# Kernel tuning notes

Hardware: AMD Instinct MI355X
Metric: run time of the kernel (lower is better)

## Reference

```python
import jax, jax.numpy as jnp
import numpy as np

WS = (7, 7)          # window size
SS = (3, 3)          # shift size
NUM_HEADS = 6


def _relative_position_index(ws):
    ch, cw = np.meshgrid(np.arange(ws[0]), np.arange(ws[1]), indexing='ij')
    coords = np.stack([ch, cw]).reshape(2, -1)           # [2, N]
    rel = coords[:, :, None] - coords[:, None, :]        # [2, N, N]
    rel = rel.transpose(1, 2, 0)
    rel[:, :, 0] += ws[0] - 1
    rel[:, :, 1] += ws[1] - 1
    rel[:, :, 0] *= 2 * ws[1] - 1
    return rel.sum(-1).reshape(-1)                       # [N*N]


def _shift_mask(pad_H, pad_W, ws, ss):
    # per-window additive mask [num_windows, N, N], -100 across shift regions
    img = np.zeros((pad_H, pad_W))
    h_slices = ((0, -ws[0]), (-ws[0], -ss[0]), (-ss[0], None))
    w_slices = ((0, -ws[1]), (-ws[1], -ss[1]), (-ss[1], None))
    cnt = 0
    for h in h_slices:
        for w in w_slices:
            img[h[0]:h[1], w[0]:w[1]] = cnt
            cnt += 1
    m = img.reshape(pad_H // ws[0], ws[0], pad_W // ws[1], ws[1])
    m = m.transpose(0, 2, 1, 3).reshape(-1, ws[0] * ws[1])   # [nW, N]
    diff = m[:, None, :] - m[:, :, None]
    return np.where(diff != 0, -100.0, 0.0).astype(np.float32)


def setup_inputs() -> dict:
    key = jax.random.key(0)
    ks = jax.random.split(key, 6)
    B, H, W, C = 16, 112, 112, 192
    return {
        'x': jax.random.normal(ks[0], (B, H, W, C), jnp.float32),
        'qkv_w': jax.random.normal(ks[1], (3 * C, C), jnp.float32) * (C ** -0.5),
        'qkv_b': jax.random.normal(ks[2], (3 * C,), jnp.float32) * 0.02,
        'proj_w': jax.random.normal(ks[3], (C, C), jnp.float32) * (C ** -0.5),
        'proj_b': jax.random.normal(ks[4], (C,), jnp.float32) * 0.02,
        'rel_bias_table': jax.random.normal(ks[5], ((2 * WS[0] - 1) * (2 * WS[1] - 1), NUM_HEADS), jnp.float32) * 0.02,
    }


def reference(x, qkv_w, qkv_b, proj_w, proj_b, rel_bias_table):
    B, H, W, C = x.shape
    ws, ss = WS, SS
    N = ws[0] * ws[1]
    hd = C // NUM_HEADS

    pad_r = (ws[1] - W % ws[1]) % ws[1]
    pad_b = (ws[0] - H % ws[0]) % ws[0]
    x = jnp.pad(x, ((0, 0), (0, pad_b), (0, pad_r), (0, 0)))
    pad_H, pad_W = H + pad_b, W + pad_r
    ss = (0 if ws[0] >= pad_H else ss[0], 0 if ws[1] >= pad_W else ss[1])
    shifted = sum(ss) > 0

    if shifted:
        x = jnp.roll(x, (-ss[0], -ss[1]), axis=(1, 2))

    nWh, nWw = pad_H // ws[0], pad_W // ws[1]
    nW = nWh * nWw
    # window partition -> [B*nW, N, C]
    x = x.reshape(B, nWh, ws[0], nWw, ws[1], C).transpose(0, 1, 3, 2, 4, 5).reshape(B * nW, N, C)

    qkv = x @ qkv_w.T + qkv_b                               # [B*nW, N, 3C]
    qkv = qkv.reshape(B * nW, N, 3, NUM_HEADS, hd).transpose(2, 0, 3, 1, 4)
    q, k, v = qkv[0], qkv[1], qkv[2]                        # [B*nW, h, N, hd]

    q = q * (hd ** -0.5)
    attn = jnp.einsum('whnd,whmd->whnm', q, k)              # [B*nW, h, N, N]

    rel_idx = _relative_position_index(ws)
    rel_bias = rel_bias_table[rel_idx].reshape(N, N, NUM_HEADS).transpose(2, 0, 1)
    attn = attn + rel_bias[None]

    if shifted:
        mask = jnp.asarray(_shift_mask(pad_H, pad_W, ws, ss))   # [nW, N, N]
        attn = attn.reshape(B, nW, NUM_HEADS, N, N) + mask[None, :, None]
        attn = attn.reshape(B * nW, NUM_HEADS, N, N)

    attn = jax.nn.softmax(attn, axis=-1)
    out = jnp.einsum('whnm,whmd->whnd', attn, v)            # [B*nW, h, N, hd]
    out = out.transpose(0, 2, 1, 3).reshape(B * nW, N, C)
    out = out @ proj_w.T + proj_b

    out = out.reshape(B, nWh, nWw, ws[0], ws[1], C).transpose(0, 1, 3, 2, 4, 5).reshape(B, pad_H, pad_W, C)
    if shifted:
        out = jnp.roll(out, (ss[0], ss[1]), axis=(1, 2))
    return out[:, :H, :W, :]
```

## Files before the change

### kernel.cpp

```cpp
#include <hip/hip_runtime.h>

typedef __bf16 bf16_t;
typedef __bf16 bf16x8 __attribute__((ext_vector_type(8)));
typedef __bf16 bf16x4 __attribute__((ext_vector_type(4)));
typedef float  f32x4  __attribute__((ext_vector_type(4)));

#define MFMA16(a,b,c) __builtin_amdgcn_mfma_f32_16x16x32_bf16((a),(b),(c),0,0,0)

#define REG_STRIDE 200
#define VT_STRIDE  68
#define REG_ELEMS  13056
#define SC_STRIDE  40
#define SC_CHUNK   640
#define BT_OFF     (REG_ELEMS + 6 * SC_CHUNK)
#define SMEM_ELEMS (BT_OFF + 1014)

#define WPROJ_OFF 110592
#define WTOTAL    147456

__global__ void convert_w_kernel(const float* __restrict__ qkv_w,
                                 const float* __restrict__ proj_w,
                                 bf16_t* __restrict__ wb) {
    const int i = (blockIdx.x * 256 + threadIdx.x) * 4;
    float4 f;
    if (i < WPROJ_OFF) f = *(const float4*)(qkv_w + i);
    else               f = *(const float4*)(proj_w + (i - WPROJ_OFF));
    bf16x4 v;
    v[0] = (bf16_t)f.x; v[1] = (bf16_t)f.y; v[2] = (bf16_t)f.z; v[3] = (bf16_t)f.w;
    *(bf16x4*)(wb + i) = v;
}

__device__ __forceinline__ void gemm64x32(const bf16_t* __restrict__ xa,
                                          const bf16_t* __restrict__ w0,
                                          const bf16_t* __restrict__ w1,
                                          f32x4 acc[4][2]) {
    bf16x8 b0 = *(const bf16x8*)(w0);
    bf16x8 b1 = *(const bf16x8*)(w1);
    bf16x8 n0 = *(const bf16x8*)(w0 + 32);
    bf16x8 n1 = *(const bf16x8*)(w1 + 32);
    #pragma unroll
    for (int ks = 0; ks < 6; ++ks) {
        bf16x8 m0, m1;
        if (ks < 4) {
            m0 = *(const bf16x8*)(w0 + (ks + 2) * 32);
            m1 = *(const bf16x8*)(w1 + (ks + 2) * 32);
        }
        #pragma unroll
        for (int mi = 0; mi < 4; ++mi) {
            const bf16x8 afr = *(const bf16x8*)(xa + (mi * 16) * REG_STRIDE + ks * 32);
            acc[mi][0] = MFMA16(afr, b0, acc[mi][0]);
            acc[mi][1] = MFMA16(afr, b1, acc[mi][1]);
        }
        b0 = n0; b1 = n1; n0 = m0; n1 = m1;
    }
}

__global__ __launch_bounds__(384, 5)
void swin_fused_kernel(const float* __restrict__ x,
                       const bf16_t* __restrict__ wbuf,
                       const float* __restrict__ qkv_b,
                       const float* __restrict__ proj_b,
                       const float* __restrict__ tbl,
                       float* __restrict__ out)
{
    __shared__ __align__(16) bf16_t smem[SMEM_ELEMS];
    bf16_t* region = smem;
    bf16_t* bt     = smem + BT_OFF;

    const int tid    = threadIdx.x;
    const int lane   = tid & 63;
    const int wave   = tid >> 6;
    const int lanelo = lane & 15;
    const int quad   = lane >> 4;

    bf16_t* sc = smem + REG_ELEMS + wave * SC_CHUNK;

    const int blk = blockIdx.x;
    const int b   = blk >> 8;
    const int wh  = (blk >> 4) & 15;
    const int ww  = blk & 15;
    const int rowbase = wh * 7 + 3;
    const int colbase = ww * 7 + 3;

    for (int i = tid; i < 1014; i += 384) bt[i] = (bf16_t)tbl[i];

    for (int idx = tid; idx < 64 * 48; idx += 384) {
        const int t  = idx / 48;
        const int c4 = (idx - t * 48) * 4;
        bf16x4 v4;
        if (t < 49) {
            int gr = rowbase + t / 7;  if (gr >= 112) gr -= 112;
            int gc = colbase + t % 7;  if (gc >= 112) gc -= 112;
            const float4 f = *(const float4*)(x + (((long)b * 112 + gr) * 112 + gc) * 192 + c4);
            v4[0] = (bf16_t)f.x; v4[1] = (bf16_t)f.y;
            v4[2] = (bf16_t)f.z; v4[3] = (bf16_t)f.w;
        } else {
            v4[0] = (bf16_t)0.0f; v4[1] = (bf16_t)0.0f;
            v4[2] = (bf16_t)0.0f; v4[3] = (bf16_t)0.0f;
        }
        *(bf16x4*)(region + t * REG_STRIDE + c4) = v4;
    }
    __syncthreads();

    const int h = wave;
    const bf16_t* xa = region + lanelo * REG_STRIDE + quad * 8;

    bf16x8 qa[4], kb[4];
    f32x4  vacc[4][2];
    {
        {
            const bf16_t* wb = wbuf + (0 * 192 + h * 32) * 192;
            f32x4 acc[4][2] = {};
            gemm64x32(xa, wb + lanelo * 192 + quad * 8, wb + (16 + lanelo) * 192 + quad * 8, acc);
            const float bias0 = qkv_b[0 * 192 + h * 32 + lanelo];
            const float bias1 = qkv_b[0 * 192 + h * 32 + 16 + lanelo];
            #pragma unroll
            for (int mi = 0; mi < 4; ++mi) {
                #pragma unroll
                for (int r = 0; r < 4; ++r) {
                    sc[(quad * 4 + r) * SC_STRIDE + lanelo]      = (bf16_t)(acc[mi][0][r] + bias0);
                    sc[(quad * 4 + r) * SC_STRIDE + 16 + lanelo] = (bf16_t)(acc[mi][1][r] + bias1);
                }
                qa[mi] = *(const bf16x8*)(sc + lanelo * SC_STRIDE + quad * 8);
            }
        }
        {
            const bf16_t* wb = wbuf + (1 * 192 + h * 32) * 192;
            f32x4 acc[4][2] = {};
            gemm64x32(xa, wb + lanelo * 192 + quad * 8, wb + (16 + lanelo) * 192 + quad * 8, acc);
            const float bias0 = qkv_b[1 * 192 + h * 32 + lanelo];
            const float bias1 = qkv_b[1 * 192 + h * 32 + 16 + lanelo];
            #pragma unroll
            for (int mi = 0; mi < 4; ++mi) {
                #pragma unroll
                for (int r = 0; r < 4; ++r) {
                    sc[(quad * 4 + r) * SC_STRIDE + lanelo]      = (bf16_t)(acc[mi][0][r] + bias0);
                    sc[(quad * 4 + r) * SC_STRIDE + 16 + lanelo] = (bf16_t)(acc[mi][1][r] + bias1);
                }
                kb[mi] = *(const bf16x8*)(sc + lanelo * SC_STRIDE + quad * 8);
            }
        }
        {
            const bf16_t* wb = wbuf + (2 * 192 + h * 32) * 192;
            f32x4 acc[4][2] = {};
            gemm64x32(xa, wb + lanelo * 192 + quad * 8, wb + (16 + lanelo) * 192 + quad * 8, acc);
            #pragma unroll
            for (int mi = 0; mi < 4; ++mi) {
                vacc[mi][0] = acc[mi][0];
                vacc[mi][1] = acc[mi][1];
            }
        }
    }
    __syncthreads();

    {
        const float bias0 = qkv_b[2 * 192 + h * 32 + lanelo];
        const float bias1 = qkv_b[2 * 192 + h * 32 + 16 + lanelo];
        #pragma unroll
        for (int mi = 0; mi < 4; ++mi)
            #pragma unroll
            for (int r = 0; r < 4; ++r) {
                const int tok = quad * 4 + r + 16 * mi;
                region[(h * 32 + lanelo) * VT_STRIDE + tok]      = (bf16_t)(vacc[mi][0][r] + bias0);
                region[(h * 32 + 16 + lanelo) * VT_STRIDE + tok] = (bf16_t)(vacc[mi][1][r] + bias1);
            }
    }

    f32x4 o_[4][2] = {};
    {
        const float scale = 0.17677669529663687f;

        int kvalid[4], kch[4], kcw[4], kid[4];
        #pragma unroll
        for (int ni = 0; ni < 4; ++ni) {
            const int col = ni * 16 + lanelo;
            kvalid[ni] = (col < 49);
            const int cc = kvalid[ni] ? col : 48;
            kch[ni] = cc / 7; kcw[ni] = cc - kch[ni] * 7;
            const int gr = wh * 7 + kch[ni], gc = ww * 7 + kcw[ni];
            kid[ni] = (gr < 105 ? 0 : (gr < 109 ? 1 : 2)) * 3 + (gc < 105 ? 0 : (gc < 109 ? 1 : 2));
        }

        const bf16x8 bv00 = *(const bf16x8*)(region + (h * 32 + lanelo) * VT_STRIDE + quad * 8);
        const bf16x8 bv01 = *(const bf16x8*)(region + (h * 32 + 16 + lanelo) * VT_STRIDE + quad * 8);
        const bf16x8 bv10 = *(const bf16x8*)(region + (h * 32 + lanelo) * VT_STRIDE + 32 + quad * 8);
        const bf16x8 bv11 = *(const bf16x8*)(region + (h * 32 + 16 + lanelo) * VT_STRIDE + 32 + quad * 8);

        #pragma unroll
        for (int mi = 0; mi < 4; ++mi) {
            f32x4 s[4];
            #pragma unroll
            for (int ni = 0; ni < 4; ++ni) {
                f32x4 z = {0.f, 0.f, 0.f, 0.f};
                s[ni] = MFMA16(qa[mi], kb[ni], z);
            }
            #pragma unroll
            for (int r = 0; r < 4; ++r) {
                const int row = mi * 16 + quad * 4 + r;
                const int rq  = (row < 49) ? row : 48;
                const int rh  = rq / 7, rw = rq - (rq / 7) * 7;
                const int gqr = wh * 7 + rh, gqc = ww * 7 + rw;
                const int idq = (gqr < 105 ? 0 : (gqr < 109 ? 1 : 2)) * 3 + (gqc < 105 ? 0 : (gqc < 109 ? 1 : 2));
                #pragma unroll
                for (int ni = 0; ni < 4; ++ni) {
                    float v;
                    if (kvalid[ni]) {
                        const int bidx = ((rh - kch[ni] + 6) * 13 + (rw - kcw[ni] + 6)) * 6 + h;
                        v = s[ni][r] * scale + (float)bt[bidx];
                        if (idq != kid[ni]) v -= 100.0f;
                    } else {
                        v = -1e30f;
                    }
                    s[ni][r] = v;
                }
                float m0 = fmaxf(fmaxf(s[0][r], s[1][r]), fmaxf(s[2][r], s[3][r]));
                m0 = fmaxf(m0, __shfl_xor(m0, 1));
                m0 = fmaxf(m0, __shfl_xor(m0, 2));
                m0 = fmaxf(m0, __shfl_xor(m0, 4));
                m0 = fmaxf(m0, __shfl_xor(m0, 8));
                float sum = 0.f;
                #pragma unroll
                for (int ni = 0; ni < 4; ++ni) {
                    const float e = __expf(s[ni][r] - m0);
                    s[ni][r] = e;
                    sum += e;
                }
                sum += __shfl_xor(sum, 1);
                sum += __shfl_xor(sum, 2);
                sum += __shfl_xor(sum, 4);
                sum += __shfl_xor(sum, 8);
                const float rinv = 1.0f / sum;
                sc[(quad * 4 + r) * SC_STRIDE + lanelo]      = (bf16_t)(s[0][r] * rinv);
                sc[(quad * 4 + r) * SC_STRIDE + 16 + lanelo] = (bf16_t)(s[1][r] * rinv);
                s[2][r] *= rinv;
                s[3][r] *= rinv;
            }
            {
                const bf16x8 ap = *(const bf16x8*)(sc + lanelo * SC_STRIDE + quad * 8);
                o_[mi][0] = MFMA16(ap, bv00, o_[mi][0]);
                o_[mi][1] = MFMA16(ap, bv01, o_[mi][1]);
            }
            #pragma unroll
            for (int r = 0; r < 4; ++r) {
                sc[(quad * 4 + r) * SC_STRIDE + lanelo]      = (bf16_t)s[2][r];
                sc[(quad * 4 + r) * SC_STRIDE + 16 + lanelo] = (bf16_t)s[3][r];
            }
            {
                const bf16x8 ap = *(const bf16x8*)(sc + lanelo * SC_STRIDE + quad * 8);
                o_[mi][0] = MFMA16(ap, bv10, o_[mi][0]);
                o_[mi][1] = MFMA16(ap, bv11, o_[mi][1]);
            }
        }
    }
    __syncthreads();

    #pragma unroll
    for (int mi = 0; mi < 4; ++mi)
        #pragma unroll
        for (int r = 0; r < 4; ++r) {
            const int row = quad * 4 + r + 16 * mi;
            region[row * REG_STRIDE + h * 32 + lanelo]      = (bf16_t)(o_[mi][0][r]);
            region[row * REG_STRIDE + h * 32 + 16 + lanelo] = (bf16_t)(o_[mi][1][r]);
        }
    __syncthreads();

    {
        const bf16_t* wb = wbuf + WPROJ_OFF + (wave * 32) * 192;
        f32x4 acc[4][2] = {};
        gemm64x32(xa, wb + lanelo * 192 + quad * 8, wb + (16 + lanelo) * 192 + quad * 8, acc);
        const int o0 = wave * 32 + lanelo;
        const int o1 = wave * 32 + 16 + lanelo;
        const float pb0 = proj_b[o0];
        const float pb1 = proj_b[o1];
        #pragma unroll
        for (int mi = 0; mi < 4; ++mi)
            #pragma unroll
            for (int r = 0; r < 4; ++r) {
                const int row = quad * 4 + r + 16 * mi;
                if (row < 49) {
                    int gr = rowbase + row / 7;  if (gr >= 112) gr -= 112;
                    int gc = colbase + row % 7;  if (gc >= 112) gc -= 112;
                    float* op = out + (((long)b * 112 + gr) * 112 + gc) * 192;
                    op[o0] = acc[mi][0][r] + pb0;
                    op[o1] = acc[mi][1][r] + pb1;
                }
            }
    }
}

extern "C" void kernel_launch(void* const* d_in, const int* in_sizes, int n_in,
                              void* d_out, int out_size, void* d_ws, size_t ws_size,
                              hipStream_t stream) {
    const float* x      = (const float*)d_in[0];
    const float* qkv_w  = (const float*)d_in[1];
    const float* qkv_b  = (const float*)d_in[2];
    const float* proj_w = (const float*)d_in[3];
    const float* proj_b = (const float*)d_in[4];
    const float* tbl    = (const float*)d_in[5];
    bf16_t* wbuf = (bf16_t*)d_ws;

    convert_w_kernel<<<144, 256, 0, stream>>>(qkv_w, proj_w, wbuf);
    swin_fused_kernel<<<4096, 384, 0, stream>>>(x, wbuf, qkv_b, proj_b, tbl,
                                                (float*)d_out);
}
```

Before: 580.6 us.

## Process two windows per block to reuse weight fragments across windows

Each block now handles two adjacent windows instead of one, so every weight fragment loaded from global memory feeds MFMAs for both windows. The QKV projection order is also reordered (V first, then K, then Q) so register lifetimes shrink. The cost is doubled shared memory and register use per block; launch bounds drop from 5 to 3 blocks per CU and the grid is halved, which lowers occupancy and latency hiding.

```diff
diff --git a/kernel.cpp b/kernel.cpp
--- a/kernel.cpp
+++ b/kernel.cpp
@@ -12,11 +12,11 @@
 #define REG_ELEMS  13056
 #define SC_STRIDE  40
 #define SC_CHUNK   640
-#define BT_OFF     (REG_ELEMS + 6 * SC_CHUNK)
+#define SC_OFF     (2 * REG_ELEMS)
+#define BT_OFF     (SC_OFF + 6 * SC_CHUNK)
 #define SMEM_ELEMS (BT_OFF + 1014)
 
 #define WPROJ_OFF 110592
-#define WTOTAL    147456
 
 __global__ void convert_w_kernel(const float* __restrict__ qkv_w,
                                  const float* __restrict__ proj_w,
@@ -30,10 +30,11 @@
     *(bf16x4*)(wb + i) = v;
 }
 
-__device__ __forceinline__ void gemm64x32(const bf16_t* __restrict__ xa,
-                                          const bf16_t* __restrict__ w0,
-                                          const bf16_t* __restrict__ w1,
-                                          f32x4 acc[4][2]) {
+__device__ __forceinline__ void gemm2(const bf16_t* __restrict__ xaA,
+                                      const bf16_t* __restrict__ xaB,
+                                      const bf16_t* __restrict__ w0,
+                                      const bf16_t* __restrict__ w1,
+                                      f32x4 accA[4][2], f32x4 accB[4][2]) {
     bf16x8 b0 = *(const bf16x8*)(w0);
     bf16x8 b1 = *(const bf16x8*)(w1);
     bf16x8 n0 = *(const bf16x8*)(w0 + 32);
@@ -47,15 +48,35 @@
         }
         #pragma unroll
         for (int mi = 0; mi < 4; ++mi) {
-            const bf16x8 afr = *(const bf16x8*)(xa + (mi * 16) * REG_STRIDE + ks * 32);
-            acc[mi][0] = MFMA16(afr, b0, acc[mi][0]);
-            acc[mi][1] = MFMA16(afr, b1, acc[mi][1]);
+            const bf16x8 aA = *(const bf16x8*)(xaA + (mi * 16) * REG_STRIDE + ks * 32);
+            accA[mi][0] = MFMA16(aA, b0, accA[mi][0]);
+            accA[mi][1] = MFMA16(aA, b1, accA[mi][1]);
+        }
+        #pragma unroll
+        for (int mi = 0; mi < 4; ++mi) {
+            const bf16x8 aB = *(const bf16x8*)(xaB + (mi * 16) * REG_STRIDE + ks * 32);
+            accB[mi][0] = MFMA16(aB, b0, accB[mi][0]);
+            accB[mi][1] = MFMA16(aB, b1, accB[mi][1]);
         }
         b0 = n0; b1 = n1; n0 = m0; n1 = m1;
     }
 }
 
-__global__ __launch_bounds__(384, 5)
+__device__ __forceinline__ void roundtrip(bf16_t* __restrict__ sc, int lanelo, int quad,
+                                          const f32x4 acc[4][2], float bias0, float bias1,
+                                          bf16x8 outfr[4]) {
+    #pragma unroll
+    for (int mi = 0; mi < 4; ++mi) {
+        #pragma unroll
+        for (int r = 0; r < 4; ++r) {
+            sc[(quad * 4 + r) * SC_STRIDE + lanelo]      = (bf16_t)(acc[mi][0][r] + bias0);
+            sc[(quad * 4 + r) * SC_STRIDE + 16 + lanelo] = (bf16_t)(acc[mi][1][r] + bias1);
+        }
+        outfr[mi] = *(const bf16x8*)(sc + lanelo * SC_STRIDE + quad * 8);
+    }
+}
+
+__global__ __launch_bounds__(384, 3)
 void swin_fused_kernel(const float* __restrict__ x,
                        const bf16_t* __restrict__ wbuf,
                        const float* __restrict__ qkv_b,
@@ -64,8 +85,7 @@
                        float* __restrict__ out)
 {
     __shared__ __align__(16) bf16_t smem[SMEM_ELEMS];
-    bf16_t* region = smem;
-    bf16_t* bt     = smem + BT_OFF;
+    bf16_t* bt = smem + BT_OFF;
 
     const int tid    = threadIdx.x;
     const int lane   = tid & 63;
@@ -73,218 +93,230 @@
     const int lanelo = lane & 15;
     const int quad   = lane >> 4;
 
-    bf16_t* sc = smem + REG_ELEMS + wave * SC_CHUNK;
+    bf16_t* sc = smem + SC_OFF + wave * SC_CHUNK;
 
     const int blk = blockIdx.x;
-    const int b   = blk >> 8;
-    const int wh  = (blk >> 4) & 15;
-    const int ww  = blk & 15;
-    const int rowbase = wh * 7 + 3;
-    const int colbase = ww * 7 + 3;
+    const int b   = blk >> 7;
+    const int wh  = (blk >> 3) & 15;
+    const int ww0 = (blk & 7) * 2;
+    const int rowbase  = wh * 7 + 3;
+    const int colbase0 = ww0 * 7 + 3;
 
     for (int i = tid; i < 1014; i += 384) bt[i] = (bf16_t)tbl[i];
 
-    for (int idx = tid; idx < 64 * 48; idx += 384) {
-        const int t  = idx / 48;
-        const int c4 = (idx - t * 48) * 4;
-        bf16x4 v4;
-        if (t < 49) {
-            int gr = rowbase + t / 7;  if (gr >= 112) gr -= 112;
-            int gc = colbase + t % 7;  if (gc >= 112) gc -= 112;
-            const float4 f = *(const float4*)(x + (((long)b * 112 + gr) * 112 + gc) * 192 + c4);
-            v4[0] = (bf16_t)f.x; v4[1] = (bf16_t)f.y;
-            v4[2] = (bf16_t)f.z; v4[3] = (bf16_t)f.w;
-        } else {
-            v4[0] = (bf16_t)0.0f; v4[1] = (bf16_t)0.0f;
-            v4[2] = (bf16_t)0.0f; v4[3] = (bf16_t)0.0f;
-        }
-        *(bf16x4*)(region + t * REG_STRIDE + c4) = v4;
+    #pragma unroll
+    for (int w = 0; w < 2; ++w) {
+        bf16_t* reg = smem + w * REG_ELEMS;
+        const int cb = colbase0 + w * 7;
+        #pragma unroll 4
+        for (int it = 0; it < 8; ++it) {
+            const int idx = tid + it * 384;
+            const int t  = idx / 48;
+            const int c4 = (idx - t * 48) * 4;
+            bf16x4 v4;
+            if (t < 49) {
+                int gr = rowbase + t / 7;  if (gr >= 112) gr -= 112;
+                int gc = cb + t % 7;       if (gc >= 112) gc -= 112;
+                const float4 f = *(const float4*)(x + (((long)b * 112 + gr) * 112 + gc) * 192 + c4);
+                v4[0] = (bf16_t)f.x; v4[1] = (bf16_t)f.y;
+                v4[2] = (bf16_t)f.z; v4[3] = (bf16_t)f.w;
+            } else {
+                v4[0] = (bf16_t)0.0f; v4[1] = (bf16_t)0.0f;
+                v4[2] = (bf16_t)0.0f; v4[3] = (bf16_t)0.0f;
+            }
+            *(bf16x4*)(reg + t * REG_STRIDE + c4) = v4;
+        }
     }
     __syncthreads();
 
     const int h = wave;
-    const bf16_t* xa = region + lanelo * REG_STRIDE + quad * 8;
-
-    bf16x8 qa[4], kb[4];
-    f32x4  vacc[4][2];
-    {
-        {
-            const bf16_t* wb = wbuf + (0 * 192 + h * 32) * 192;
-            f32x4 acc[4][2] = {};
-            gemm64x32(xa, wb + lanelo * 192 + quad * 8, wb + (16 + lanelo) * 192 + quad * 8, acc);
-            const float bias0 = qkv_b[0 * 192 + h * 32 + lanelo];
-            const float bias1 = qkv_b[0 * 192 + h * 32 + 16 + lanelo];
-            #pragma unroll
-            for (int mi = 0; mi < 4; ++mi) {
+    const bf16_t* xaA = smem + lanelo * REG_STRIDE + quad * 8;
+    const bf16_t* xaB = smem + REG_ELEMS + lanelo * REG_STRIDE + quad * 8;
+
+    f32x4  vacc[2][4][2] = {};
+    bf16x8 kb[2][4], qa[2][4];
+    {
+        const bf16_t* wb = wbuf + (2 * 192 + h * 32) * 192;
+        gemm2(xaA, xaB, wb + lanelo * 192 + quad * 8, wb + (16 + lanelo) * 192 + quad * 8,
+              vacc[0], vacc[1]);
+    }
+    {
+        const bf16_t* wb = wbuf + (1 * 192 + h * 32) * 192;
+        f32x4 tacc[2][4][2] = {};
+        gemm2(xaA, xaB, wb + lanelo * 192 + quad * 8, wb + (16 + lanelo) * 192 + quad * 8,
+              tacc[0], tacc[1]);
+        const float b0 = qkv_b[192 + h * 32 + lanelo];
+        const float b1 = qkv_b[192 + h * 32 + 16 + lanelo];
+        roundtrip(sc, lanelo, quad, tacc[0], b0, b1, kb[0]);
+        roundtrip(sc, lanelo, quad, tacc[1], b0, b1, kb[1]);
+    }
+    {
+        const bf16_t* wb = wbuf + (0 * 192 + h * 32) * 192;
+        f32x4 tacc[2][4][2] = {};
+        gemm2(xaA, xaB, wb + lanelo * 192 + quad * 8, wb + (16 + lanelo) * 192 + quad * 8,
+              tacc[0], tacc[1]);
+        const float b0 = qkv_b[h * 32 + lanelo];
+        const float b1 = qkv_b[h * 32 + 16 + lanelo];
+        roundtrip(sc, lanelo, quad, tacc[0], b0, b1, qa[0]);
+        roundtrip(sc, lanelo, quad, tacc[1], b0, b1, qa[1]);
+    }
+    __syncthreads();
+
+    {
+        const float b0 = qkv_b[2 * 192 + h * 32 + lanelo];
+        const float b1 = qkv_b[2 * 192 + h * 32 + 16 + lanelo];
+        #pragma unroll
+        for (int w = 0; w < 2; ++w) {
+            bf16_t* reg = smem + w * REG_ELEMS;
+            #pragma unroll
+            for (int mi = 0; mi < 4; ++mi)
                 #pragma unroll
                 for (int r = 0; r < 4; ++r) {
-                    sc[(quad * 4 + r) * SC_STRIDE + lanelo]      = (bf16_t)(acc[mi][0][r] + bias0);
-                    sc[(quad * 4 + r) * SC_STRIDE + 16 + lanelo] = (bf16_t)(acc[mi][1][r] + bias1);
-                }
-                qa[mi] = *(const bf16x8*)(sc + lanelo * SC_STRIDE + quad * 8);
-            }
-        }
-        {
-            const bf16_t* wb = wbuf + (1 * 192 + h * 32) * 192;
-            f32x4 acc[4][2] = {};
-            gemm64x32(xa, wb + lanelo * 192 + quad * 8, wb + (16 + lanelo) * 192 + quad * 8, acc);
-            const float bias0 = qkv_b[1 * 192 + h * 32 + lanelo];
-            const float bias1 = qkv_b[1 * 192 + h * 32 + 16 + lanelo];
-            #pragma unroll
-            for (int mi = 0; mi < 4; ++mi) {
-                #pragma unroll
-                for (int r = 0; r < 4; ++r) {
-                    sc[(quad * 4 + r) * SC_STRIDE + lanelo]      = (bf16_t)(acc[mi][0][r] + bias0);
-                    sc[(quad * 4 + r) * SC_STRIDE + 16 + lanelo] = (bf16_t)(acc[mi][1][r] + bias1);
-                }
-                kb[mi] = *(const bf16x8*)(sc + lanelo * SC_STRIDE + quad * 8);
-            }
-        }
-        {
-            const bf16_t* wb = wbuf + (2 * 192 + h * 32) * 192;
-            f32x4 acc[4][2] = {};
-            gemm64x32(xa, wb + lanelo * 192 + quad * 8, wb + (16 + lanelo) * 192 + quad * 8, acc);
-            #pragma unroll
-            for (int mi = 0; mi < 4; ++mi) {
-                vacc[mi][0] = acc[mi][0];
-                vacc[mi][1] = acc[mi][1];
-            }
-        }
-    }
-    __syncthreads();
-
-    {
-        const float bias0 = qkv_b[2 * 192 + h * 32 + lanelo];
-        const float bias1 = qkv_b[2 * 192 + h * 32 + 16 + lanelo];
-        #pragma unroll
-        for (int mi = 0; mi < 4; ++mi)
-            #pragma unroll
-            for (int r = 0; r < 4; ++r) {
-                const int tok = quad * 4 + r + 16 * mi;
-                region[(h * 32 + lanelo) * VT_STRIDE + tok]      = (bf16_t)(vacc[mi][0][r] + bias0);
-                region[(h * 32 + 16 + lanelo) * VT_STRIDE + tok] = (bf16_t)(vacc[mi][1][r] + bias1);
-            }
-    }
-
-    f32x4 o_[4][2] = {};
+                    const int tok = quad * 4 + r + 16 * mi;
+                    reg[(h * 32 + lanelo) * VT_STRIDE + tok]      = (bf16_t)(vacc[w][mi][0][r] + b0);
+                    reg[(h * 32 + 16 + lanelo) * VT_STRIDE + tok] = (bf16_t)(vacc[w][mi][1][r] + b1);
+                }
+        }
+    }
+
+    f32x4 o_[2][4][2] = {};
     {
         const float scale = 0.17677669529663687f;
 
-        int kvalid[4], kch[4], kcw[4], kid[4];
+        int kvalid[4], kch[4], kcw[4];
         #pragma unroll
         for (int ni = 0; ni < 4; ++ni) {
             const int col = ni * 16 + lanelo;
             kvalid[ni] = (col < 49);
             const int cc = kvalid[ni] ? col : 48;
             kch[ni] = cc / 7; kcw[ni] = cc - kch[ni] * 7;
-            const int gr = wh * 7 + kch[ni], gc = ww * 7 + kcw[ni];
-            kid[ni] = (gr < 105 ? 0 : (gr < 109 ? 1 : 2)) * 3 + (gc < 105 ? 0 : (gc < 109 ? 1 : 2));
-        }
-
-        const bf16x8 bv00 = *(const bf16x8*)(region + (h * 32 + lanelo) * VT_STRIDE + quad * 8);
-        const bf16x8 bv01 = *(const bf16x8*)(region + (h * 32 + 16 + lanelo) * VT_STRIDE + quad * 8);
-        const bf16x8 bv10 = *(const bf16x8*)(region + (h * 32 + lanelo) * VT_STRIDE + 32 + quad * 8);
-        const bf16x8 bv11 = *(const bf16x8*)(region + (h * 32 + 16 + lanelo) * VT_STRIDE + 32 + quad * 8);
-
-        #pragma unroll
-        for (int mi = 0; mi < 4; ++mi) {
-            f32x4 s[4];
+        }
+
+        #pragma unroll
+        for (int w = 0; w < 2; ++w) {
+            const bf16_t* reg = smem + w * REG_ELEMS;
+            const int wwl = ww0 + w;
+            int kid[4];
             #pragma unroll
             for (int ni = 0; ni < 4; ++ni) {
-                f32x4 z = {0.f, 0.f, 0.f, 0.f};
-                s[ni] = MFMA16(qa[mi], kb[ni], z);
+                const int gr = wh * 7 + kch[ni], gc = wwl * 7 + kcw[ni];
+                kid[ni] = (gr < 105 ? 0 : (gr < 109 ? 1 : 2)) * 3 + (gc < 105 ? 0 : (gc < 109 ? 1 : 2));
             }
+
+            const bf16x8 bv00 = *(const bf16x8*)(reg + (h * 32 + lanelo) * VT_STRIDE + quad * 8);
+            const bf16x8 bv01 = *(const bf16x8*)(reg + (h * 32 + 16 + lanelo) * VT_STRIDE + quad * 8);
+            const bf16x8 bv10 = *(const bf16x8*)(reg + (h * 32 + lanelo) * VT_STRIDE + 32 + quad * 8);
+            const bf16x8 bv11 = *(const bf16x8*)(reg + (h * 32 + 16 + lanelo) * VT_STRIDE + 32 + quad * 8);
+
+            #pragma unroll
+            for (int mi = 0; mi < 4; ++mi) {
+                f32x4 s[4];
+                #pragma unroll
+                for (int ni = 0; ni < 4; ++ni) {
+                    f32x4 z = {0.f, 0.f, 0.f, 0.f};
+                    s[ni] = MFMA16(qa[w][mi], kb[w][ni], z);
+                }
+                #pragma unroll
+                for (int r = 0; r < 4; ++r) {
+                    const int row = mi * 16 + quad * 4 + r;
+                    const int rq  = (row < 49) ? row : 48;
+                    const int rh  = rq / 7, rw = rq - (rq / 7) * 7;
+                    const int gqr = wh * 7 + rh, gqc = wwl * 7 + rw;
+                    const int idq = (gqr < 105 ? 0 : (gqr < 109 ? 1 : 2)) * 3 + (gqc < 105 ? 0 : (gqc < 109 ? 1 : 2));
+                    #pragma unroll
+                    for (int ni = 0; ni < 4; ++ni) {
+                        float v;
+                        if (kvalid[ni]) {
+                            const int bidx = ((rh - kch[ni] + 6) * 13 + (rw - kcw[ni] + 6)) * 6 + h;
+                            v = s[ni][r] * scale + (float)bt[bidx];
+                            if (idq != kid[ni]) v -= 100.0f;
+                        } else {
+                            v = -1e30f;
+                        }
+                        s[ni][r] = v;
+                    }
+                    float m0 = fmaxf(fmaxf(s[0][r], s[1][r]), fmaxf(s[2][r], s[3][r]));
+                    m0 = fmaxf(m0, __shfl_xor(m0, 1));
+                    m0 = fmaxf(m0, __shfl_xor(m0, 2));
+                    m0 = fmaxf(m0, __shfl_xor(m0, 4));
+                    m0 = fmaxf(m0, __shfl_xor(m0, 8));
+                    float sum = 0.f;
+                    #pragma unroll
+                    for (int ni = 0; ni < 4; ++ni) {
+                        const float e = __expf(s[ni][r] - m0);
+                        s[ni][r] = e;
+                        sum += e;
+                    }
+                    sum += __shfl_xor(sum, 1);
+                    sum += __shfl_xor(sum, 2);
+                    sum += __shfl_xor(sum, 4);
+                    sum += __shfl_xor(sum, 8);
+                    const float rinv = 1.0f / sum;
+                    sc[(quad * 4 + r) * SC_STRIDE + lanelo]      = (bf16_t)(s[0][r] * rinv);
+                    sc[(quad * 4 + r) * SC_STRIDE + 16 + lanelo] = (bf16_t)(s[1][r] * rinv);
+                    s[2][r] *= rinv;
+                    s[3][r] *= rinv;
+                }
+                {
+                    const bf16x8 ap = *(const bf16x8*)(sc + lanelo * SC_STRIDE + quad * 8);
+                    o_[w][mi][0] = MFMA16(ap, bv00, o_[w][mi][0]);
+                    o_[w][mi][1] = MFMA16(ap, bv01, o_[w][mi][1]);
+                }
+                #pragma unroll
+                for (int r = 0; r < 4; ++r) {
+                    sc[(quad * 4 + r) * SC_STRIDE + lanelo]      = (bf16_t)s[2][r];
+                    sc[(quad * 4 + r) * SC_STRIDE + 16 + lanelo] = (bf16_t)s[3][r];
+                }
+                {
+                    const bf16x8 ap = *(const bf16x8*)(sc + lanelo * SC_STRIDE + quad * 8);
+                    o_[w][mi][0] = MFMA16(ap, bv10, o_[w][mi][0]);
+                    o_[w][mi][1] = MFMA16(ap, bv11, o_[w][mi][1]);
+                }
+            }
+        }
+    }
+    __syncthreads();
+
+    #pragma unroll
+    for (int w = 0; w < 2; ++w) {
+        bf16_t* reg = smem + w * REG_ELEMS;
+        #pragma unroll
+        for (int mi = 0; mi < 4; ++mi)
             #pragma unroll
             for (int r = 0; r < 4; ++r) {
-                const int row = mi * 16 + quad * 4 + r;
-                const int rq  = (row < 49) ? row : 48;
-                const int rh  = rq / 7, rw = rq - (rq / 7) * 7;
-                const int gqr = wh * 7 + rh, gqc = ww * 7 + rw;
-                const int idq = (gqr < 105 ? 0 : (gqr < 109 ? 1 : 2)) * 3 + (gqc < 105 ? 0 : (gqc < 109 ? 1 : 2));
-                #pragma unroll
-                for (int ni = 0; ni < 4; ++ni) {
-                    float v;
-                    if (kvalid[ni]) {
-                        const int bidx = ((rh - kch[ni] + 6) * 13 + (rw - kcw[ni] + 6)) * 6 + h;
-                        v = s[ni][r] * scale + (float)bt[bidx];
-                        if (idq != kid[ni]) v -= 100.0f;
-                    } else {
-                        v = -1e30f;
-                    }
-                    s[ni][r] = v;
-                }
-                float m0 = fmaxf(fmaxf(s[0][r], s[1][r]), fmaxf(s[2][r], s[3][r]));
-                m0 = fmaxf(m0, __shfl_xor(m0, 1));
-                m0 = fmaxf(m0, __shfl_xor(m0, 2));
-                m0 = fmaxf(m0, __shfl_xor(m0, 4));
-                m0 = fmaxf(m0, __shfl_xor(m0, 8));
-                float sum = 0.f;
-                #pragma unroll
-                for (int ni = 0; ni < 4; ++ni) {
-                    const float e = __expf(s[ni][r] - m0);
-                    s[ni][r] = e;
-                    sum += e;
-                }
-                sum += __shfl_xor(sum, 1);
-                sum += __shfl_xor(sum, 2);
-                sum += __shfl_xor(sum, 4);
-                sum += __shfl_xor(sum, 8);
-                const float rinv = 1.0f / sum;
-                sc[(quad * 4 + r) * SC_STRIDE + lanelo]      = (bf16_t)(s[0][r] * rinv);
-                sc[(quad * 4 + r) * SC_STRIDE + 16 + lanelo] = (bf16_t)(s[1][r] * rinv);
-                s[2][r] *= rinv;
-                s[3][r] *= rinv;
+                const int row = quad * 4 + r + 16 * mi;
+                reg[row * REG_STRIDE + h * 32 + lanelo]      = (bf16_t)(o_[w][mi][0][r]);
+                reg[row * REG_STRIDE + h * 32 + 16 + lanelo] = (bf16_t)(o_[w][mi][1][r]);
             }
-            {
-                const bf16x8 ap = *(const bf16x8*)(sc + lanelo * SC_STRIDE + quad * 8);
-                o_[mi][0] = MFMA16(ap, bv00, o_[mi][0]);
-                o_[mi][1] = MFMA16(ap, bv01, o_[mi][1]);
-            }
-            #pragma unroll
-            for (int r = 0; r < 4; ++r) {
-                sc[(quad * 4 + r) * SC_STRIDE + lanelo]      = (bf16_t)s[2][r];
-                sc[(quad * 4 + r) * SC_STRIDE + 16 + lanelo] = (bf16_t)s[3][r];
-            }
-            {
-                const bf16x8 ap = *(const bf16x8*)(sc + lanelo * SC_STRIDE + quad * 8);
-                o_[mi][0] = MFMA16(ap, bv10, o_[mi][0]);
-                o_[mi][1] = MFMA16(ap, bv11, o_[mi][1]);
-            }
-        }
     }
     __syncthreads();
 
-    #pragma unroll
-    for (int mi = 0; mi < 4; ++mi)
-        #pragma unroll
-        for (int r = 0; r < 4; ++r) {
-            const int row = quad * 4 + r + 16 * mi;
-            region[row * REG_STRIDE + h * 32 + lanelo]      = (bf16_t)(o_[mi][0][r]);
-            region[row * REG_STRIDE + h * 32 + 16 + lanelo] = (bf16_t)(o_[mi][1][r]);
-        }
-    __syncthreads();
-
-    {
-        const bf16_t* wb = wbuf + WPROJ_OFF + (wave * 32) * 192;
-        f32x4 acc[4][2] = {};
-        gemm64x32(xa, wb + lanelo * 192 + quad * 8, wb + (16 + lanelo) * 192 + quad * 8, acc);
-        const int o0 = wave * 32 + lanelo;
-        const int o1 = wave * 32 + 16 + lanelo;
+    {
+        const bf16_t* wb = wbuf + WPROJ_OFF + (h * 32) * 192;
+        f32x4 pacc[2][4][2] = {};
+        gemm2(xaA, xaB, wb + lanelo * 192 + quad * 8, wb + (16 + lanelo) * 192 + quad * 8,
+              pacc[0], pacc[1]);
+        const int o0 = h * 32 + lanelo;
+        const int o1 = o0 + 16;
         const float pb0 = proj_b[o0];
         const float pb1 = proj_b[o1];
         #pragma unroll
-        for (int mi = 0; mi < 4; ++mi)
-            #pragma unroll
-            for (int r = 0; r < 4; ++r) {
-                const int row = quad * 4 + r + 16 * mi;
-                if (row < 49) {
-                    int gr = rowbase + row / 7;  if (gr >= 112) gr -= 112;
-                    int gc = colbase + row % 7;  if (gc >= 112) gc -= 112;
-                    float* op = out + (((long)b * 112 + gr) * 112 + gc) * 192;
-                    op[o0] = acc[mi][0][r] + pb0;
-                    op[o1] = acc[mi][1][r] + pb1;
-                }
-            }
+        for (int w = 0; w < 2; ++w) {
+            const int cb = colbase0 + w * 7;
+            #pragma unroll
+            for (int mi = 0; mi < 4; ++mi)
+                #pragma unroll
+                for (int r = 0; r < 4; ++r) {
+                    const int row = quad * 4 + r + 16 * mi;
+                    if (row < 49) {
+                        int gr = rowbase + row / 7;  if (gr >= 112) gr -= 112;
+                        int gc = cb + row % 7;       if (gc >= 112) gc -= 112;
+                        float* op = out + (((long)b * 112 + gr) * 112 + gc) * 192;
+                        op[o0] = pacc[w][mi][0][r] + pb0;
+                        op[o1] = pacc[w][mi][1][r] + pb1;
+                    }
+                }
+        }
     }
 }
 
@@ -300,6 +332,6 @@
     bf16_t* wbuf = (bf16_t*)d_ws;
 
     convert_w_kernel<<<144, 256, 0, stream>>>(qkv_w, proj_w, wbuf);
-    swin_fused_kernel<<<4096, 384, 0, stream>>>(x, wbuf, qkv_b, proj_b, tbl,
+    swin_fused_kernel<<<2048, 384, 0, stream>>>(x, wbuf, qkv_b, proj_b, tbl,
                                                 (float*)d_out);
 }
```

Result: slower. 789.5 us (+36.0%).
